# Kernel tuning notes

Hardware: AMD Instinct MI355X
Metric: run time of the kernel (lower is better)

## Reference

```python
import jax, jax.numpy as jnp
import numpy as np

VOCAB = 50257
EMB = 512
HID = 1024
H = HID // 2  # per-direction hidden
TAGS = 24
START = 22
STOP = 23
SEQ = 4096
NEG = -10000.0


def setup_inputs() -> dict:
    key = jax.random.key(0)
    ks = jax.random.split(key, 16)
    s = 1.0 / np.sqrt(H)
    u = lambda k, shp: jax.random.uniform(k, shp, jnp.float32, -s, s)
    sentence = jax.random.randint(ks[0], (SEQ,), 0, VOCAB)
    emb = jax.random.normal(ks[1], (VOCAB, EMB), jnp.float32)
    w_ih_f = u(ks[2], (4 * H, EMB)); w_hh_f = u(ks[3], (4 * H, H))
    b_ih_f = u(ks[4], (4 * H,));    b_hh_f = u(ks[5], (4 * H,))
    w_ih_b = u(ks[6], (4 * H, EMB)); w_hh_b = u(ks[7], (4 * H, H))
    b_ih_b = u(ks[8], (4 * H,));    b_hh_b = u(ks[9], (4 * H,))
    w_tag = u(ks[10], (TAGS, HID)); b_tag = u(ks[11], (TAGS,))
    transitions = jax.random.normal(ks[12], (TAGS, TAGS), jnp.float32)
    transitions = transitions.at[START, :].set(NEG).at[:, STOP].set(NEG)
    h0 = jax.random.normal(ks[13], (2, H), jnp.float32)  # [dir, H]
    c0 = jax.random.normal(ks[14], (2, H), jnp.float32)
    return dict(sentence=sentence, emb=emb,
                w_ih_f=w_ih_f, w_hh_f=w_hh_f, b_ih_f=b_ih_f, b_hh_f=b_hh_f,
                w_ih_b=w_ih_b, w_hh_b=w_hh_b, b_ih_b=b_ih_b, b_hh_b=b_hh_b,
                w_tag=w_tag, b_tag=b_tag, transitions=transitions, h0=h0, c0=c0)


def _lstm_dir(x, w_ih, w_hh, b_ih, b_hh, h, c, reverse):
    # x: [T, EMB]; precompute input projections once
    xg = x @ w_ih.T + (b_ih + b_hh)  # [T, 4H]
    def step(carry, xt):
        h, c = carry
        g = xt + h @ w_hh.T
        i, f, gg, o = jnp.split(g, 4)
        i = jax.nn.sigmoid(i); f = jax.nn.sigmoid(f)
        gg = jnp.tanh(gg);     o = jax.nn.sigmoid(o)
        c = f * c + i * gg
        h = o * jnp.tanh(c)
        return (h, c), h
    _, hs = jax.lax.scan(step, (h, c), xg, reverse=reverse)
    return hs  # [T, H]


def reference(sentence, emb, w_ih_f, w_hh_f, b_ih_f, b_hh_f,
              w_ih_b, w_hh_b, b_ih_b, b_hh_b, w_tag, b_tag,
              transitions, h0, c0):
    x = emb[sentence]  # [T, EMB]
    hf = _lstm_dir(x, w_ih_f, w_hh_f, b_ih_f, b_hh_f, h0[0], c0[0], False)
    hb = _lstm_dir(x, w_ih_b, w_hh_b, b_ih_b, b_hh_b, h0[1], c0[1], True)
    lstm_out = jnp.concatenate([hf, hb], axis=-1)          # [T, HID]
    feats = lstm_out @ w_tag.T + b_tag                     # [T, TAGS]

    # Viterbi: max-plus recursion over tags, vectorized per timestep
    fv0 = jnp.full((TAGS,), NEG, jnp.float32).at[START].set(0.0)
    def vstep(fv, feat):
        scores = transitions + fv[None, :]                 # [next, prev]
        bp = jnp.argmax(scores, axis=1)
        return jnp.max(scores, axis=1) + feat, bp
    fv, bps = jax.lax.scan(vstep, fv0, feats)              # bps: [T, TAGS]

    terminal = fv + transitions[STOP]
    best = jnp.argmax(terminal)
    path_score = terminal[best]

    def btstep(tag, bp):
        prev = bp[tag]
        return prev, prev
    _, ys = jax.lax.scan(btstep, best, bps, reverse=True)  # ys[t] = tag at t-1; ys[0]==START
    best_path = jnp.concatenate([ys[1:], best[None]]).astype(jnp.int32)
    return path_score, best_path
```

## Files before the change

### kernel.cpp

```cpp
#include <hip/hip_runtime.h>
#include <cstdint>
#include <cstddef>

#define T_SEQ 4096
#define EMB_D 512
#define HDIM 512
#define G4 2048
#define NTAGS 24
#define START_TAG 22
#define STOP_TAG 23
#define NEGV -10000.0f
#define NBLK 32
#define HSLICE 16
#define SENT 0xFFFFFFFFu

__global__ __launch_bounds__(256) void gemm_xg_kernel(
    const int* __restrict__ sent, const float* __restrict__ emb,
    const float* __restrict__ w_ih_f, const float* __restrict__ b_ih_f, const float* __restrict__ b_hh_f,
    const float* __restrict__ w_ih_b, const float* __restrict__ b_ih_b, const float* __restrict__ b_hh_b,
    float* __restrict__ xg)
{
    const int dir = blockIdx.z;
    const float* W  = dir ? w_ih_b : w_ih_f;
    const float* bi = dir ? b_ih_b : b_ih_f;
    const float* bh = dir ? b_hh_b : b_hh_f;
    const int m0 = blockIdx.y * 64;
    const int n0 = blockIdx.x * 64;
    const int tid = threadIdx.x;

    __shared__ __attribute__((aligned(16))) float As[32][64];
    __shared__ __attribute__((aligned(16))) float Bs[32][64];

    const int lrow = tid >> 2;
    const int lk   = (tid & 3) * 8;

    const int srow = sent[m0 + lrow];
    const float* aptr = emb + (size_t)srow * EMB_D + lk;
    const float* bptr = W   + (size_t)(n0 + lrow) * EMB_D + lk;

    const int ty = tid >> 4;
    const int tx = tid & 15;

    float acc[4][4];
    #pragma unroll
    for (int i = 0; i < 4; ++i)
        #pragma unroll
        for (int j = 0; j < 4; ++j) acc[i][j] = 0.f;

    for (int kk = 0; kk < EMB_D; kk += 32) {
        float4 a0 = *(const float4*)(aptr + kk);
        float4 a1 = *(const float4*)(aptr + kk + 4);
        float4 b0 = *(const float4*)(bptr + kk);
        float4 b1 = *(const float4*)(bptr + kk + 4);
        __syncthreads();
        As[lk+0][lrow]=a0.x; As[lk+1][lrow]=a0.y; As[lk+2][lrow]=a0.z; As[lk+3][lrow]=a0.w;
        As[lk+4][lrow]=a1.x; As[lk+5][lrow]=a1.y; As[lk+6][lrow]=a1.z; As[lk+7][lrow]=a1.w;
        Bs[lk+0][lrow]=b0.x; Bs[lk+1][lrow]=b0.y; Bs[lk+2][lrow]=b0.z; Bs[lk+3][lrow]=b0.w;
        Bs[lk+4][lrow]=b1.x; Bs[lk+5][lrow]=b1.y; Bs[lk+6][lrow]=b1.z; Bs[lk+7][lrow]=b1.w;
        __syncthreads();
        #pragma unroll
        for (int k = 0; k < 32; ++k) {
            float4 av = *(const float4*)&As[k][ty*4];
            float4 bv = *(const float4*)&Bs[k][tx*4];
            acc[0][0]+=av.x*bv.x; acc[0][1]+=av.x*bv.y; acc[0][2]+=av.x*bv.z; acc[0][3]+=av.x*bv.w;
            acc[1][0]+=av.y*bv.x; acc[1][1]+=av.y*bv.y; acc[1][2]+=av.y*bv.z; acc[1][3]+=av.y*bv.w;
            acc[2][0]+=av.z*bv.x; acc[2][1]+=av.z*bv.y; acc[2][2]+=av.z*bv.z; acc[2][3]+=av.z*bv.w;
            acc[3][0]+=av.w*bv.x; acc[3][1]+=av.w*bv.y; acc[3][2]+=av.w*bv.z; acc[3][3]+=av.w*bv.w;
        }
    }
    #pragma unroll
    for (int i = 0; i < 4; ++i) {
        const int t = m0 + ty*4 + i;
        float* crow = xg + ((size_t)dir*T_SEQ + t) * G4 + n0 + tx*4;
        #pragma unroll
        for (int j = 0; j < 4; ++j) {
            const int jg = n0 + tx*4 + j;
            crow[j] = acc[i][j] + bi[jg] + bh[jg];
        }
    }
}

__global__ __attribute__((amdgpu_waves_per_eu(2, 2))) __launch_bounds__(512)
void bilstm_kernel(
    const float* __restrict__ w_hh_f, const float* __restrict__ w_hh_b,
    const float* __restrict__ h0, const float* __restrict__ c0,
    const float* __restrict__ xg,
    uint32_t* __restrict__ h_hist,
    int* __restrict__ claim)
{
    uint32_t xcc;
    asm volatile("s_getreg_b32 %0, hwreg(HW_REG_XCC_ID)" : "=s"(xcc));
    xcc &= 7u;

    __shared__ int rank_s;
    if (threadIdx.x == 0)
        rank_s = __hip_atomic_fetch_add(&claim[xcc], 1, __ATOMIC_RELAXED,
                                        __HIP_MEMORY_SCOPE_AGENT);
    __syncthreads();
    const int rank = rank_s;

    int dir;
    if (xcc == 0) dir = 0;
    else if (xcc == 1) dir = 1;
    else return;
    if (rank >= NBLK) return;
    const int b = rank;

    const int tid = threadIdx.x;
    const int q   = tid >> 6;
    const int rl  = tid & 63;
    const int g2  = rl >> 4;
    const int hu  = rl & 15;
    const int row = g2 * HDIM + b * HSLICE + hu;

    const float* Wrow = (dir ? w_hh_b : w_hh_f) + (size_t)row * HDIM + q * 64;
    float w[64];
    #pragma unroll
    for (int j = 0; j < 16; ++j) {
        float4 v = ((const float4*)Wrow)[j];
        w[4*j+0]=v.x; w[4*j+1]=v.y; w[4*j+2]=v.z; w[4*j+3]=v.w;
    }
    #pragma unroll
    for (int i = 0; i < 64; ++i) asm volatile("" : "+v"(w[i]));

    __shared__ __attribute__((aligned(16))) float hbuf[512];
    __shared__ float part[512];

    float c = (tid < HSLICE) ? c0[dir*HDIM + b*HSLICE + tid] : 0.f;

    const float* xgd = xg + (size_t)dir * T_SEQ * G4;
    uint32_t* hh = h_hist + (size_t)dir * T_SEQ * HDIM;

    for (int idx = 0; idx < T_SEQ; ++idx) {
        const int t = dir ? (T_SEQ - 1 - idx) : idx;
        float xv = 0.f;
        if (tid < 64) xv = xgd[(size_t)t * G4 + row];

        if (idx == 0) {
            hbuf[tid] = h0[dir*HDIM + tid];
        } else {
            const int tprev = dir ? (t + 1) : (t - 1);
            const uint32_t* wp = hh + (size_t)tprev*HDIM + tid;
            uint32_t u;
            do {
                u = __hip_atomic_load(wp, __ATOMIC_RELAXED, __HIP_MEMORY_SCOPE_AGENT);
            } while (u == SENT);
            union { uint32_t u; float f; } cv; cv.u = u;
            hbuf[tid] = cv.f;
        }
        __syncthreads();

        float s = 0.f;
        const float4* hb4 = (const float4*)&hbuf[q*64];
        #pragma unroll
        for (int j = 0; j < 16; ++j) {
            float4 hv = hb4[j];
            s += w[4*j+0]*hv.x + w[4*j+1]*hv.y + w[4*j+2]*hv.z + w[4*j+3]*hv.w;
        }
        part[tid] = s;
        __syncthreads();

        if (tid < 64) {
            float g = xv;
            #pragma unroll
            for (int qq = 0; qq < 8; ++qq) g += part[qq*64 + tid];
            g = (g2 == 2) ? tanhf(g) : 1.f/(1.f + expf(-g));
            float iv = __shfl(g, hu);
            float fg = __shfl(g, hu + 16);
            float gv = __shfl(g, hu + 32);
            float ov = __shfl(g, hu + 48);
            if (tid < HSLICE) {
                c = fg*c + iv*gv;
                union { float f; uint32_t u; } hb; hb.f = ov * tanhf(c);
                __hip_atomic_store(hh + (size_t)t*HDIM + b*HSLICE + tid, hb.u,
                                   __ATOMIC_RELAXED, __HIP_MEMORY_SCOPE_AGENT);
            }
        }
    }
}

__global__ __launch_bounds__(256) void feats_kernel(
    const float* __restrict__ h_hist, const float* __restrict__ w_tag,
    const float* __restrict__ b_tag, float* __restrict__ feats)
{
    const int t = blockIdx.x;
    const int tid = threadIdx.x;
    __shared__ __attribute__((aligned(16))) float h[1024];
    __shared__ float partl[192];
    for (int i = tid; i < 512; i += 256) {
        h[i]     = h_hist[(size_t)t*HDIM + i];
        h[512+i] = h_hist[(size_t)T_SEQ*HDIM + (size_t)t*HDIM + i];
    }
    __syncthreads();
    if (tid < 192) {
        const int tag = tid >> 3, p = tid & 7;
        const float* wr = w_tag + (size_t)tag*1024 + p*128;
        const float* hp = h + p*128;
        float s = 0.f;
        #pragma unroll 8
        for (int j = 0; j < 128; ++j) s += wr[j]*hp[j];
        partl[tid] = s;
    }
    __syncthreads();
    if (tid < NTAGS) {
        float s = b_tag[tid];
        #pragma unroll
        for (int p = 0; p < 8; ++p) s += partl[tid*8+p];
        feats[(size_t)t*NTAGS + tid] = s;
    }
}

__global__ void viterbi_fwd_kernel(
    const float* __restrict__ feats, const float* __restrict__ trans,
    float* __restrict__ d_out, unsigned char* __restrict__ bp,
    int* __restrict__ best_tag)
{
    const int lane = threadIdx.x;
    const bool act = lane < NTAGS;
    float tr[NTAGS];
    #pragma unroll
    for (int p = 0; p < NTAGS; ++p)
        tr[p] = act ? trans[lane*NTAGS + p] : NEGV;

    float fv = (lane == START_TAG) ? 0.f : NEGV;
    __shared__ float fvs[NTAGS];
    __shared__ float term[NTAGS];

    float ftn = act ? feats[lane] : 0.f;
    for (int t = 0; t < T_SEQ; ++t) {
        if (act) fvs[lane] = fv;
        __syncthreads();
        float ft = ftn;
        if (act && t + 1 < T_SEQ) ftn = feats[(size_t)(t+1)*NTAGS + lane];
        float bestv = -3.4e38f;
        int argp = 0;
        #pragma unroll
        for (int p = 0; p < NTAGS; ++p) {
            float sc = tr[p] + fvs[p];
            if (sc > bestv) { bestv = sc; argp = p; }
        }
        __syncthreads();
        fv = bestv + ft;
        if (act) bp[(size_t)t*NTAGS + lane] = (unsigned char)argp;
    }
    if (act) { fv += trans[STOP_TAG*NTAGS + lane]; term[lane] = fv; }
    __syncthreads();
    if (lane == 0) {
        float bv = term[0]; int bi = 0;
        #pragma unroll
        for (int p = 1; p < NTAGS; ++p) if (term[p] > bv) { bv = term[p]; bi = p; }
        d_out[0] = bv;
        *best_tag = bi;
    }
}

__global__ void bt_compose_kernel(const unsigned char* __restrict__ bp,
                                  unsigned char* __restrict__ segmap)
{
    const int s = blockIdx.x;
    const int tid = threadIdx.x;
    __shared__ __attribute__((aligned(16))) unsigned char lbp[64*NTAGS];
    const uint32_t* src = (const uint32_t*)(bp + (size_t)s * 64 * NTAGS);
    uint32_t* dst = (uint32_t*)lbp;
    #pragma unroll
    for (int i = 0; i < 6; ++i) dst[tid + 64*i] = src[tid + 64*i];
    __syncthreads();
    if (tid < NTAGS) {
        int m = tid;
        for (int tt = 63; tt >= 0; --tt) m = lbp[tt*NTAGS + m];
        segmap[s*NTAGS + tid] = (unsigned char)m;
    }
}

__global__ void bt_final_kernel(const unsigned char* __restrict__ segmap,
                                const int* __restrict__ best_tag,
                                int* __restrict__ end_tags)
{
    if (threadIdx.x == 0) {
        int tag = *best_tag;
        end_tags[63] = tag;
        for (int s = 63; s >= 1; --s) {
            tag = segmap[s*NTAGS + tag];
            end_tags[s-1] = tag;
        }
    }
}

__global__ void bt_write_kernel(const unsigned char* __restrict__ bp,
                                const int* __restrict__ end_tags,
                                float* __restrict__ out_path)
{
    const int s = blockIdx.x;
    const int tid = threadIdx.x;
    __shared__ __attribute__((aligned(16))) unsigned char lbp[64*NTAGS];
    const uint32_t* src = (const uint32_t*)(bp + (size_t)s * 64 * NTAGS);
    uint32_t* dst = (uint32_t*)lbp;
    #pragma unroll
    for (int i = 0; i < 6; ++i) dst[tid + 64*i] = src[tid + 64*i];
    __syncthreads();
    if (tid == 0) {
        int tag = end_tags[s];
        out_path[s*64 + 63] = (float)tag;
        for (int tt = 63; tt >= 1; --tt) {
            tag = lbp[tt*NTAGS + tag];
            out_path[s*64 + tt - 1] = (float)tag;
        }
    }
}

extern "C" void kernel_launch(void* const* d_in, const int* in_sizes, int n_in,
                              void* d_out, int out_size, void* d_ws, size_t ws_size,
                              hipStream_t stream)
{
    const int*   sent   = (const int*)d_in[0];
    const float* emb    = (const float*)d_in[1];
    const float* w_ih_f = (const float*)d_in[2];
    const float* w_hh_f = (const float*)d_in[3];
    const float* b_ih_f = (const float*)d_in[4];
    const float* b_hh_f = (const float*)d_in[5];
    const float* w_ih_b = (const float*)d_in[6];
    const float* w_hh_b = (const float*)d_in[7];
    const float* b_ih_b = (const float*)d_in[8];
    const float* b_hh_b = (const float*)d_in[9];
    const float* w_tag  = (const float*)d_in[10];
    const float* b_tag  = (const float*)d_in[11];
    const float* trans  = (const float*)d_in[12];
    const float* h0     = (const float*)d_in[13];
    const float* c0     = (const float*)d_in[14];
    float* out = (float*)d_out;

    char* ws = (char*)d_ws;
    size_t off = 0;
    auto alloc = [&](size_t bytes) {
        char* p = ws + off; off += (bytes + 255) & ~(size_t)255; return p;
    };
    float* xg      = (float*)alloc((size_t)2*T_SEQ*G4*sizeof(float));
    uint32_t* h_hist = (uint32_t*)alloc((size_t)2*T_SEQ*HDIM*sizeof(float));
    float* feats   = (float*)alloc((size_t)T_SEQ*NTAGS*sizeof(float));
    unsigned char* bp     = (unsigned char*)alloc((size_t)T_SEQ*NTAGS);
    unsigned char* segmap = (unsigned char*)alloc(64*NTAGS);
    int* best_tag = (int*)alloc(sizeof(int));
    int* end_tags = (int*)alloc(64*sizeof(int));
    int* claim    = (int*)alloc(8*sizeof(int));

    if (off > ws_size) {
        hipMemsetAsync(d_out, 0xFF, 4, stream);
        return;
    }

    hipMemsetAsync(h_hist, 0xFF, (size_t)2*T_SEQ*HDIM*sizeof(float), stream);
    hipMemsetAsync(claim, 0, 8*sizeof(int), stream);

    dim3 gg(G4/64, T_SEQ/64, 2);
    gemm_xg_kernel<<<gg, 256, 0, stream>>>(sent, emb,
        w_ih_f, b_ih_f, b_hh_f, w_ih_b, b_ih_b, b_hh_b, xg);
    bilstm_kernel<<<512, 512, 0, stream>>>(w_hh_f, w_hh_b, h0, c0, xg, h_hist, claim);
    feats_kernel<<<T_SEQ, 256, 0, stream>>>((const float*)h_hist, w_tag, b_tag, feats);
    viterbi_fwd_kernel<<<1, 64, 0, stream>>>(feats, trans, out, bp, best_tag);
    bt_compose_kernel<<<64, 64, 0, stream>>>(bp, segmap);
    bt_final_kernel<<<1, 64, 0, stream>>>(segmap, best_tag, end_tags);
    bt_write_kernel<<<64, 64, 0, stream>>>(bp, end_tags, out + 1);
}
```

Baseline: 8.741 ms.

## Broadcast hidden state via readlane and prefetch next-step input gates

Each wave now reads the hidden-state values it needs from its own lanes with readlane, instead of staging them through shared memory. This removes one block-wide barrier per recurrent step. The partial-sum buffer is double-buffered so the one remaining barrier is enough to avoid write-after-read hazards between steps. The xg value for the next timestep is also loaded one iteration early to hide global-load latency on the serial critical path. The cost is 64 scalar readlanes per step in place of LDS vector reads.

Result: no change. 8.850 ms (+1.2%).

```diff
diff --git a/kernel.cpp b/kernel.cpp
--- a/kernel.cpp
+++ b/kernel.cpp
@@ -123,21 +123,31 @@
     #pragma unroll
     for (int i = 0; i < 64; ++i) asm volatile("" : "+v"(w[i]));
 
-    __shared__ __attribute__((aligned(16))) float hbuf[512];
-    __shared__ float part[512];
+    __shared__ __attribute__((aligned(16))) float part[2][512];
 
     float c = (tid < HSLICE) ? c0[dir*HDIM + b*HSLICE + tid] : 0.f;
 
     const float* xgd = xg + (size_t)dir * T_SEQ * G4;
     uint32_t* hh = h_hist + (size_t)dir * T_SEQ * HDIM;
 
+    float xv_cur = 0.f;
+    if (tid < 64) {
+        const int t0 = dir ? (T_SEQ - 1) : 0;
+        xv_cur = xgd[(size_t)t0 * G4 + row];
+    }
+
     for (int idx = 0; idx < T_SEQ; ++idx) {
         const int t = dir ? (T_SEQ - 1 - idx) : idx;
-        float xv = 0.f;
-        if (tid < 64) xv = xgd[(size_t)t * G4 + row];
-
+
+        float xv_nxt = 0.f;
+        if (tid < 64 && idx + 1 < T_SEQ) {
+            const int tn = dir ? (t - 1) : (t + 1);
+            xv_nxt = xgd[(size_t)tn * G4 + row];
+        }
+
+        float hv;
         if (idx == 0) {
-            hbuf[tid] = h0[dir*HDIM + tid];
+            hv = h0[dir*HDIM + tid];
         } else {
             const int tprev = dir ? (t + 1) : (t - 1);
             const uint32_t* wp = hh + (size_t)tprev*HDIM + tid;
@@ -145,25 +155,28 @@
             do {
                 u = __hip_atomic_load(wp, __ATOMIC_RELAXED, __HIP_MEMORY_SCOPE_AGENT);
             } while (u == SENT);
-            union { uint32_t u; float f; } cv; cv.u = u;
-            hbuf[tid] = cv.f;
-        }
-        __syncthreads();
-
+            union { uint32_t uu; float f; } cv; cv.uu = u;
+            hv = cv.f;
+        }
+
+        const uint32_t hvu = __float_as_uint(hv);
         float s = 0.f;
-        const float4* hb4 = (const float4*)&hbuf[q*64];
         #pragma unroll
         for (int j = 0; j < 16; ++j) {
-            float4 hv = hb4[j];
-            s += w[4*j+0]*hv.x + w[4*j+1]*hv.y + w[4*j+2]*hv.z + w[4*j+3]*hv.w;
-        }
-        part[tid] = s;
+            const float h0v = __uint_as_float((uint32_t)__builtin_amdgcn_readlane((int)hvu, 4*j+0));
+            const float h1v = __uint_as_float((uint32_t)__builtin_amdgcn_readlane((int)hvu, 4*j+1));
+            const float h2v = __uint_as_float((uint32_t)__builtin_amdgcn_readlane((int)hvu, 4*j+2));
+            const float h3v = __uint_as_float((uint32_t)__builtin_amdgcn_readlane((int)hvu, 4*j+3));
+            s += w[4*j+0]*h0v + w[4*j+1]*h1v + w[4*j+2]*h2v + w[4*j+3]*h3v;
+        }
+        part[idx & 1][tid] = s;
         __syncthreads();
 
         if (tid < 64) {
-            float g = xv;
+            float g = xv_cur;
+            const float* pb = part[idx & 1];
             #pragma unroll
-            for (int qq = 0; qq < 8; ++qq) g += part[qq*64 + tid];
+            for (int qq = 0; qq < 8; ++qq) g += pb[qq*64 + tid];
             g = (g2 == 2) ? tanhf(g) : 1.f/(1.f + expf(-g));
             float iv = __shfl(g, hu);
             float fg = __shfl(g, hu + 16);
@@ -176,6 +189,7 @@
                                    __ATOMIC_RELAXED, __HIP_MEMORY_SCOPE_AGENT);
             }
         }
+        xv_cur = xv_nxt;
     }
 }
 
```
